# Optimization experiments

Hardware: AMD Instinct MI355X
Metric: run time of the kernel (lower is better)

## Reference

```python
import jax, jax.numpy as jnp
import numpy as np

N = 8192      # number of input points
K = 16        # nsample for all kNN groupings
STRIDE = 4    # TransitionDown stride -> M = N // 4 output points


def _knn(q, p, k):
    # squared euclidean distances [m, n] -> k nearest indices per query
    d2 = jnp.sum(q * q, 1)[:, None] + jnp.sum(p * p, 1)[None, :] - 2.0 * (q @ p.T)
    return jax.lax.top_k(-d2, k)[1]


def _forward(points, We1, se1, be1, We2, se2, be2,
             Wq1, Wk1, Wv1, sa1, ba1, Wq2, Wk2, Wv2, sa2, ba2,
             Wtd, sd, bd, Wu1, su1, bu1, Wu2, su2, bu2,
             Wc1, bc1, sc, bc, Wc2, bc2):
    p = points[0]                      # [N, 3]
    n = p.shape[0]
    idx = _knn(p, p, K)                # [N, K] shared xyz-kNN (same coords every layer)

    def edge_conv(x, W, s, b):
        # DGCNN EdgeConv: concat(x_i, x_j - x_i) -> Linear -> BN(affine) -> ReLU -> max_k
        xi = x[:, None, :]
        xj = x[idx]                    # [N, K, C]
        e = jnp.concatenate([jnp.broadcast_to(xi, xj.shape), xj - xi], -1)
        h = jax.nn.relu((e @ W) * s + b)
        return h.max(axis=1)

    def graph_attn(x, Wq, Wk, Wv, s, b):
        q, kk, v = x @ Wq, x @ Wk, x @ Wv
        kj, vj = kk[idx], v[idx]       # [N, K, D]
        logits = jnp.einsum('nd,nkd->nk', q, kj) / jnp.sqrt(jnp.float32(q.shape[-1]))
        a = jax.nn.softmax(logits, axis=-1)
        y = jnp.einsum('nk,nkd->nd', a, vj)
        return jax.nn.relu(y * s + b)

    x = edge_conv(p, We1, se1, be1)            # 3 -> 64
    x = edge_conv(x, We2, se2, be2)            # 64 -> 128
    x = graph_attn(x, Wq1, Wk1, Wv1, sa1, ba1) # 128 -> 256
    x = graph_attn(x, Wq2, Wk2, Wv2, sa2, ba2) # 256 -> 512

    # TransitionDown: subsample n/stride points, group kNN with relative xyz, MLP, max-pool
    sel = jnp.arange(0, n, STRIDE)
    pm = p[sel]                                 # [M, 3]
    idx_d = _knn(pm, p, K)                      # [M, K]
    g = jnp.concatenate([p[idx_d] - pm[:, None, :], x[idx_d]], -1)  # [M, K, 3+512]
    xd = jax.nn.relu((g @ Wtd) * sd + bd).max(axis=1)               # [M, 512]

    # TransitionUp(x, o): local linear + broadcast per-cloud pooled branch (single cloud, o=[n])
    gmean = xd.mean(axis=0, keepdims=True)
    xu = jax.nn.relu((xd @ Wu1) * su1 + bu1 + (gmean @ Wu2) * su2 + bu2)  # [M, 256]

    # classifier (eval mode: dropout = identity, BN folded to affine)
    h = jax.nn.relu(((xu @ Wc1) + bc1) * sc + bc)
    return h @ Wc2 + bc2               # [M, num_classes]


def setup_inputs() -> dict:
    key = jax.random.key(0)
    ks = iter(jax.random.split(key, 64))
    def w(shape):
        return jax.random.normal(next(ks), shape, jnp.float32) / jnp.sqrt(jnp.float32(shape[0]))
    def s(d):
        return 1.0 + 0.01 * jax.random.normal(next(ks), (d,), jnp.float32)
    def b(d):
        return 0.01 * jax.random.normal(next(ks), (d,), jnp.float32)
    return {
        'points': jax.random.normal(next(ks), (1, N, 3), jnp.float32),
        'We1': w((6, 64)), 'se1': s(64), 'be1': b(64),
        'We2': w((128, 128)), 'se2': s(128), 'be2': b(128),
        'Wq1': w((128, 256)), 'Wk1': w((128, 256)), 'Wv1': w((128, 256)), 'sa1': s(256), 'ba1': b(256),
        'Wq2': w((256, 512)), 'Wk2': w((256, 512)), 'Wv2': w((256, 512)), 'sa2': s(512), 'ba2': b(512),
        'Wtd': w((515, 512)), 'sd': s(512), 'bd': b(512),
        'Wu1': w((512, 256)), 'su1': s(256), 'bu1': b(256),
        'Wu2': w((512, 256)), 'su2': s(256), 'bu2': b(256),
        'Wc1': w((256, 128)), 'bc1': b(128), 'sc': s(128), 'bc': b(128),
        'Wc2': w((128, 6)), 'bc2': b(6),
    }


def reference(points, We1, se1, be1, We2, se2, be2,
              Wq1, Wk1, Wv1, sa1, ba1, Wq2, Wk2, Wv2, sa2, ba2,
              Wtd, sd, bd, Wu1, su1, bu1, Wu2, su2, bu2,
              Wc1, bc1, sc, bc, Wc2, bc2):
    return _forward(points, We1, se1, be1, We2, se2, be2,
                    Wq1, Wk1, Wv1, sa1, ba1, Wq2, Wk2, Wv2, sa2, ba2,
                    Wtd, sd, bd, Wu1, su1, bu1, Wu2, su2, bu2,
                    Wc1, bc1, sc, bc, Wc2, bc2)
```

## Files before the change

### kernel.cpp

```cpp
#include <hip/hip_runtime.h>


#define NP 8192
#define NDOWN 2048
#define KCAP 48

typedef unsigned long long u64;
typedef __attribute__((ext_vector_type(8))) _Float16 half8;
typedef __attribute__((ext_vector_type(4))) unsigned short us4;
typedef __attribute__((ext_vector_type(8))) unsigned short ushort8;
typedef __attribute__((ext_vector_type(4))) float f32x4;

__device__ __forceinline__ bool lexless(float ad, int ai, float bd, int bi) {
  return ad < bd || (ad == bd && ai < bi);
}

__device__ __forceinline__ unsigned short f2h(float x) {
  _Float16 h = (_Float16)x;
  return __builtin_bit_cast(unsigned short, h);
}
__device__ __forceinline__ float h2f(unsigned short u) {
  return (float)__builtin_bit_cast(_Float16, u);
}

__global__ __launch_bounds__(256) void prep_points_k(const float* __restrict__ pts,
                                                     float4* __restrict__ soa) {
  int i = blockIdx.x * 256 + threadIdx.x;
  float x = pts[3 * i], y = pts[3 * i + 1], z = pts[3 * i + 2];
  soa[i] = make_float4(x, y, z, x * x + y * y + z * z);
}

__global__ __launch_bounds__(256) void wsplit_k(
    const float* __restrict__ We2, const float* __restrict__ Wq1,
    const float* __restrict__ Wk1, const float* __restrict__ Wv1,
    const float* __restrict__ Wq2, const float* __restrict__ Wk2,
    const float* __restrict__ Wv2, const float* __restrict__ Wtd,
    const float* __restrict__ Wu1, const float* __restrict__ Wc1,
    unsigned short* __restrict__ whi) {
  int t = blockIdx.x * 256 + threadIdx.x;
  float v;
  if (t < 16384) {
    int n = t >> 6, k = t & 63;
    if (n < 128) v = We2[k * 128 + n] - We2[(k + 64) * 128 + n];
    else         v = We2[(k + 64) * 128 + (n - 128)];
  } else if (t < 114688) {
    int e = t - 16384;
    int n = e >> 7, k = e & 127;
    if (n < 256)      v = Wq1[k * 256 + n];
    else if (n < 512) v = Wk1[k * 256 + (n - 256)];
    else              v = Wv1[k * 256 + (n - 512)];
  } else if (t < 507904) {
    int e = t - 114688;
    int n = e >> 8, k = e & 255;
    if (n < 512)       v = Wq2[k * 512 + n];
    else if (n < 1024) v = Wk2[k * 512 + (n - 512)];
    else               v = Wv2[k * 512 + (n - 1024)];
  } else if (t < 770048) {
    int e = t - 507904;
    int n = e >> 9, k = e & 511;
    v = Wtd[(3 + k) * 512 + n];
  } else if (t < 901120) {
    int e = t - 770048;
    int n = e >> 9, k = e & 511;
    v = Wu1[k * 256 + n];
  } else {
    int e = t - 901120;
    int n = e >> 8, k = e & 255;
    v = Wc1[k * 128 + n];
  }
  whi[t] = f2h(v);
}

__device__ __forceinline__ void bitonic_lex64(float& d, int& i, int lane) {
#pragma unroll
  for (int k = 2; k <= 64; k <<= 1) {
#pragma unroll
    for (int j = k >> 1; j >= 1; j >>= 1) {
      float od = __shfl_xor(d, j);
      int oi = __shfl_xor(i, j);
      bool takeMin = (((lane & k) == 0) == ((lane & j) == 0));
      bool less = lexless(od, oi, d, i);
      if (takeMin == less) { d = od; i = oi; }
    }
  }
}

__device__ __forceinline__ void insert1(float cd, int ci, int lane,
                                        float& td, int& ti) {
  int p = __popcll(__ballot(lexless(td, ti, cd, ci)));
  if (p < 16) {
    float ud = __shfl_up(td, 1);
    int ui = __shfl_up(ti, 1);
    float ntd = td; int nti = ti;
    if (lane > p && lane < 16) { ntd = ud; nti = ui; }
    if (lane == p) { ntd = cd; nti = ci; }
    td = ntd; ti = nti;
  }
}

__global__ __launch_bounds__(512) void knn_k(const float4* __restrict__ soa,
                                             int* __restrict__ idxout) {
  __shared__ float4 sp[2048];
  __shared__ float cb_d[8][KCAP];
  __shared__ int cb_i[8][KCAP];
  __shared__ int ccnt[8];
  const int lane = threadIdx.x & 63;
  const int wid = threadIdx.x >> 6;
  const int q = blockIdx.x * 8 + wid;
  const float4 qp = soa[q];
  const float qx2 = -2.f * qp.x, qy2 = -2.f * qp.y, qz2 = -2.f * qp.z;
  const float INF = __int_as_float(0x7f800000);
  if (lane == 0) ccnt[wid] = 0;

  float md = INF;
  int mi = 0x7fffffff;
  for (int ch = 0; ch < 4; ++ch) {
    __syncthreads();
    for (int j = 0; j < 4; ++j) {
      int e = j * 512 + threadIdx.x;
      sp[e] = soa[ch * 2048 + e];
    }
    __syncthreads();
#pragma unroll 4
    for (int c = 0; c < 32; ++c) {
      const float4 P = sp[c * 64 + lane];
      float m = fmaf(qx2, P.x, qp.w);
      m = fmaf(qy2, P.y, m);
      m = fmaf(qz2, P.z, m);
      const float d = m + P.w;
      const int gidx = ch * 2048 + c * 64 + lane;
      if (d < md) { md = d; mi = gidx; }
    }
  }
  const int own = mi;
  float sd = md; int si = mi;
  bitonic_lex64(sd, si, lane);

  float td = (lane < 16) ? sd : INF;
  int ti = (lane < 16) ? si : 0x7fffffff;
  float Td = __shfl(sd, 15); int Ti = __shfl(si, 15);
  const float tau = Td + fabsf(Td) * 1e-5f + 1e-12f;

  for (int ch = 0; ch < 4; ++ch) {
    __syncthreads();
    for (int j = 0; j < 4; ++j) {
      int e = j * 512 + threadIdx.x;
      sp[e] = soa[ch * 2048 + e];
    }
    __syncthreads();
#pragma unroll 4
    for (int c = 0; c < 32; ++c) {
      const float4 P = sp[c * 64 + lane];
      float m = fmaf(qx2, P.x, qp.w);
      m = fmaf(qy2, P.y, m);
      m = fmaf(qz2, P.z, m);
      const float d = m + P.w;
      const int gidx = ch * 2048 + c * 64 + lane;
      if (d <= tau && gidx != own) {
        int slot = atomicAdd(&ccnt[wid], 1);
        if (slot < KCAP) { cb_d[wid][slot] = d; cb_i[wid][slot] = gidx; }
      }
    }
  }
  int n = ccnt[wid];
  if (n > KCAP) {
    for (int base = 0; base < 8192; base += 64) {
      const float4 P = soa[base + lane];
      float m = fmaf(qx2, P.x, qp.w);
      m = fmaf(qy2, P.y, m);
      m = fmaf(qz2, P.z, m);
      const float d = m + P.w;
      const int gidx = base + lane;
      u64 mk = __ballot(d <= tau && gidx != own && lexless(d, gidx, Td, Ti));
      while (mk) {
        int s = (int)__builtin_ctzll(mk);
        mk &= mk - 1;
        float cd = __shfl(d, s);
        int ci = __shfl(gidx, s);
        insert1(cd, ci, lane, td, ti);
      }
      Td = __shfl(td, 15); Ti = __shfl(ti, 15);
    }
  } else {
    for (int k2 = 0; k2 < n; ++k2) {
      float cd = cb_d[wid][k2];
      int ci = cb_i[wid][k2];
      if (lexless(cd, ci, Td, Ti)) {
        insert1(cd, ci, lane, td, ti);
        Td = __shfl(td, 15); Ti = __shfl(ti, 15);
      }
    }
  }
  if (lane < 16) idxout[q * 16 + lane] = ti & 8191;
}

__global__ __launch_bounds__(256) void proj1_k(const float4* __restrict__ soa,
                                               const float* __restrict__ We1,
                                               float* __restrict__ bz1) {
  int t = blockIdx.x * 256 + threadIdx.x;
  int i = t >> 7, c = t & 127;
  float4 P = soa[i];
  float v;
  if (c < 64) {
    v = P.x * (We1[c] - We1[192 + c]) + P.y * (We1[64 + c] - We1[256 + c]) +
        P.z * (We1[128 + c] - We1[320 + c]);
  } else {
    int cc = c & 63;
    v = P.x * We1[192 + cc] + P.y * We1[256 + cc] + P.z * We1[320 + cc];
  }
  bz1[t] = v;
}

template <int C>
__global__ __launch_bounds__(256) void ec_gm_k(const float* __restrict__ bz,
                                               const int* __restrict__ idx,
                                               const float* __restrict__ s,
                                               const float* __restrict__ b,
                                               unsigned short* __restrict__ xo) {
  constexpr int C4 = C / 4;
  int t = blockIdx.x * 256 + threadIdx.x;
  int i = t / C4, q = t % C4;
  float4 base = *(const float4*)&bz[(size_t)i * (2 * C) + q * 4];
  float4 scl = *(const float4*)&s[q * 4];
  float4 bia = *(const float4*)&b[q * 4];
  float ax = 0.f, ay = 0.f, az = 0.f, aw = 0.f;
  const int* ip = idx + i * 16;
#pragma unroll
  for (int n = 0; n < 16; ++n) {
    int j = ip[n];
    float4 z = *(const float4*)&bz[(size_t)j * (2 * C) + C + q * 4];
    ax = fmaxf(ax, (base.x + z.x) * scl.x + bia.x);
    ay = fmaxf(ay, (base.y + z.y) * scl.y + bia.y);
    az = fmaxf(az, (base.z + z.z) * scl.z + bia.z);
    aw = fmaxf(aw, (base.w + z.w) * scl.w + bia.w);
  }
  us4 o;
  o[0] = f2h(ax); o[1] = f2h(ay); o[2] = f2h(az); o[3] = f2h(aw);
  *(us4*)&xo[(size_t)i * C + q * 4] = o;
}

template <int C>
__global__ __launch_bounds__(256) void attn_logits_k(const float* __restrict__ qf,
                                                     const unsigned short* __restrict__ kvb,
                                                     const int* __restrict__ idx,
                                                     float* __restrict__ aout,
                                                     float scale) {
  int i = blockIdx.x * 4 + (threadIdx.x >> 6);
  int lane = threadIdx.x & 63;
  constexpr int G = C / 256;
  float4 qv[G];
#pragma unroll
  for (int g = 0; g < G; ++g)
    qv[g] = *(const float4*)&qf[(size_t)i * C + 4 * lane + 256 * g];
  float lg[16];
#pragma unroll
  for (int n = 0; n < 16; ++n) {
    int j = idx[i * 16 + n];
    const unsigned short* kr = kvb + (size_t)j * (2 * C);
    float ssum = 0.f;
#pragma unroll
    for (int g = 0; g < G; ++g) {
      us4 kk = *(const us4*)&kr[4 * lane + 256 * g];
      ssum += qv[g].x * h2f(kk[0]) + qv[g].y * h2f(kk[1]) +
              qv[g].z * h2f(kk[2]) + qv[g].w * h2f(kk[3]);
    }
    lg[n] = ssum;
  }
#pragma unroll
  for (int n = 0; n < 16; ++n) {
    float vv = lg[n];
    for (int o = 32; o >= 1; o >>= 1) vv += __shfl_xor(vv, o);
    lg[n] = vv * scale;
  }
  float m = lg[0];
#pragma unroll
  for (int n = 1; n < 16; ++n) m = fmaxf(m, lg[n]);
  float ssum = 0.f;
#pragma unroll
  for (int n = 0; n < 16; ++n) { lg[n] = __expf(lg[n] - m); ssum += lg[n]; }
  float inv = 1.f / ssum;
  if (lane == 0) {
#pragma unroll
    for (int n = 0; n < 16; ++n) aout[i * 16 + n] = lg[n] * inv;
  }
}

template <int C>
__global__ __launch_bounds__(256) void attn_apply_k(const unsigned short* __restrict__ kvb,
                                                    const int* __restrict__ idx,
                                                    const float* __restrict__ awp,
                                                    const float* __restrict__ s,
                                                    const float* __restrict__ b,
                                                    unsigned short* __restrict__ xo) {
  constexpr int C4 = C / 4;
  int t = blockIdx.x * 256 + threadIdx.x;
  int i = t / C4, q = t % C4;
  float ax = 0.f, ay = 0.f, az = 0.f, aw2 = 0.f;
  const int* ip = idx + i * 16;
  const float* ap = awp + i * 16;
#pragma unroll
  for (int n = 0; n < 16; ++n) {
    int j = ip[n];
    float w = ap[n];
    us4 v4 = *(const us4*)&kvb[(size_t)j * (2 * C) + C + 4 * q];
    ax += w * h2f(v4[0]); ay += w * h2f(v4[1]);
    az += w * h2f(v4[2]); aw2 += w * h2f(v4[3]);
  }
  float4 scl = *(const float4*)&s[q * 4];
  float4 bia = *(const float4*)&b[q * 4];
  ax = fmaxf(ax * scl.x + bia.x, 0.f);
  ay = fmaxf(ay * scl.y + bia.y, 0.f);
  az = fmaxf(az * scl.z + bia.z, 0.f);
  aw2 = fmaxf(aw2 * scl.w + bia.w, 0.f);
  us4 o;
  o[0] = f2h(ax); o[1] = f2h(ay); o[2] = f2h(az); o[3] = f2h(aw2);
  *(us4*)&xo[(size_t)i * C + q * 4] = o;
}

__global__ __launch_bounds__(256) void down_gm_k(const float* __restrict__ vbuf,
                                                 const float4* __restrict__ soa,
                                                 const float* __restrict__ Wtd,
                                                 const int* __restrict__ idx,
                                                 const float* __restrict__ sd,
                                                 const float* __restrict__ bd,
                                                 unsigned short* __restrict__ xd) {
  int t = blockIdx.x * 256 + threadIdx.x;
  int i = t >> 7, q = t & 127;
  int qi = 4 * i;
  float4 qp = soa[qi];
  float4 w0 = *(const float4*)&Wtd[q * 4];
  float4 w1 = *(const float4*)&Wtd[512 + q * 4];
  float4 w2 = *(const float4*)&Wtd[1024 + q * 4];
  float px = qp.x * w0.x + qp.y * w1.x + qp.z * w2.x;
  float py = qp.x * w0.y + qp.y * w1.y + qp.z * w2.y;
  float pz = qp.x * w0.z + qp.y * w1.z + qp.z * w2.z;
  float pw2 = qp.x * w0.w + qp.y * w1.w + qp.z * w2.w;
  float4 scl = *(const float4*)&sd[q * 4];
  float4 bia = *(const float4*)&bd[q * 4];
  float ax = 0.f, ay = 0.f, az = 0.f, aw = 0.f;
  const int* ip = idx + qi * 16;
#pragma unroll
  for (int n = 0; n < 16; ++n) {
    int j = ip[n];
    float4 v = *(const float4*)&vbuf[(size_t)j * 512 + q * 4];
    ax = fmaxf(ax, (v.x - px) * scl.x + bia.x);
    ay = fmaxf(ay, (v.y - py) * scl.y + bia.y);
    az = fmaxf(az, (v.z - pz) * scl.z + bia.z);
    aw = fmaxf(aw, (v.w - pw2) * scl.w + bia.w);
  }
  us4 o;
  o[0] = f2h(ax); o[1] = f2h(ay); o[2] = f2h(az); o[3] = f2h(aw);
  *(us4*)&xd[(size_t)i * 512 + q * 4] = o;
}

__global__ __launch_bounds__(512) void colsum_k(const unsigned short* __restrict__ xd,
                                                float* __restrict__ part) {
  int b = blockIdx.x;
  int c = threadIdx.x;
  float s = 0.f;
  for (int r = b * 128; r < (b + 1) * 128; ++r) s += h2f(xd[(size_t)r * 512 + c]);
  part[b * 512 + c] = s;
}

__global__ __launch_bounds__(256) void gterm_k(const float* __restrict__ part,
                                               const float* __restrict__ Wu2,
                                               const float* __restrict__ su2,
                                               const float* __restrict__ bu2,
                                               float* __restrict__ gterm) {
  __shared__ float gm[512];
  int tid = threadIdx.x;
  for (int c = tid; c < 512; c += 256) {
    float s = 0.f;
#pragma unroll
    for (int b = 0; b < 16; ++b) s += part[b * 512 + c];
    gm[c] = s * (1.f / 2048.f);
  }
  __syncthreads();
  float s = 0.f;
  for (int c = 0; c < 512; ++c) s += gm[c] * Wu2[c * 256 + tid];
  gterm[tid] = s * su2[tid] + bu2[tid];
}

#define LDSROW 80
template <int MODE>
__global__ __launch_bounds__(256) void gemm_mfma(
    const unsigned short* __restrict__ A,
    const unsigned short* __restrict__ B,
    float* __restrict__ Cf, unsigned short* __restrict__ Ch,
    int M, int N, int K,
    const float4* __restrict__ soaD, const float* __restrict__ wtd,
    const float* __restrict__ s1, const float* __restrict__ b1,
    const float* __restrict__ s2, int Cq, unsigned short* __restrict__ kvb) {
  __shared__ __align__(16) char smem[2 * 128 * LDSROW];
  char* A_s = smem;
  char* B_s = smem + 128 * LDSROW;

  const int tid = threadIdx.x;
  const int lane = tid & 63;
  const int wid = tid >> 6;
  const int wm = wid >> 1, wn = wid & 1;
  const int bm = blockIdx.y * 128, bn = blockIdx.x * 128;
  const int r16 = lane & 15, kb = lane >> 4;

  f32x4 acc[4][4];
#pragma unroll
  for (int a = 0; a < 4; ++a)
#pragma unroll
    for (int b = 0; b < 4; ++b) acc[a][b] = (f32x4)(0.f);

  for (int k0 = 0; k0 < K; k0 += 32) {
    __syncthreads();
#pragma unroll
    for (int qq = 0; qq < 2; ++qq) {
      int idx8 = qq * 256 + tid;
      int row = idx8 >> 2, sq = idx8 & 3;
      size_t goA = (size_t)(bm + row) * K + k0 + sq * 8;
      size_t goB = (size_t)(bn + row) * K + k0 + sq * 8;
      ushort8 a_v = *(const ushort8*)&A[goA];
      ushort8 b_v = *(const ushort8*)&B[goB];
      *(ushort8*)(A_s + row * LDSROW + sq * 16) = a_v;
      *(ushort8*)(B_s + row * LDSROW + sq * 16) = b_v;
    }
    __syncthreads();

    half8 ah[4];
#pragma unroll
    for (int mi = 0; mi < 4; ++mi) {
      int off = (wm * 64 + mi * 16 + r16) * LDSROW + kb * 16;
      ah[mi] = *(const half8*)(A_s + off);
    }
#pragma unroll
    for (int ni = 0; ni < 4; ++ni) {
      int off = (wn * 64 + ni * 16 + r16) * LDSROW + kb * 16;
      half8 bh = *(const half8*)(B_s + off);
#pragma unroll
      for (int mi = 0; mi < 4; ++mi) {
        acc[mi][ni] = __builtin_amdgcn_mfma_f32_16x16x32_f16(ah[mi], bh, acc[mi][ni], 0, 0, 0);
      }
    }
  }

#pragma unroll
  for (int mi = 0; mi < 4; ++mi) {
#pragma unroll
    for (int ni = 0; ni < 4; ++ni) {
      int r0 = bm + wm * 64 + mi * 16 + (lane >> 4) * 4;
      int cc = bn + wn * 64 + ni * 16 + (lane & 15);
      float w0 = 0.f, w1 = 0.f, w2 = 0.f;
      if (MODE == 1) { w0 = wtd[cc]; w1 = wtd[512 + cc]; w2 = wtd[1024 + cc]; }
#pragma unroll
      for (int j = 0; j < 4; ++j) {
        float vv = acc[mi][ni][j];
        int row = r0 + j;
        if (MODE == 1) {
          float4 P = soaD[row];
          vv += P.x * w0 + P.y * w1 + P.z * w2;
        }
        if (MODE == 2) vv = fmaxf(vv * s1[cc] + b1[cc] + s2[cc], 0.f);
        if (MODE == 3) vv = fmaxf((vv + b1[cc]) * s1[cc] + s2[cc], 0.f);
        if (MODE == 2) {
          Ch[(size_t)row * N + cc] = f2h(vv);
        } else if (MODE == 4) {
          if (cc < Cq) Cf[(size_t)row * Cq + cc] = vv;
          else kvb[(size_t)row * (2 * Cq) + (cc - Cq)] = f2h(vv);
        } else {
          Cf[(size_t)row * N + cc] = vv;
        }
      }
    }
  }
}

__global__ __launch_bounds__(256) void out_k(const float* __restrict__ h,
                                             const float* __restrict__ Wc2,
                                             const float* __restrict__ bc2,
                                             float* __restrict__ out) {
  int t = blockIdx.x * 256 + threadIdx.x;
  int pair = t >> 2, kq = t & 3;
  int i = pair / 6, o = pair % 6;
  float s = 0.f;
#pragma unroll 8
  for (int m = kq * 32; m < kq * 32 + 32; ++m) s += h[i * 128 + m] * Wc2[m * 6 + o];
  s += __shfl_xor(s, 1);
  s += __shfl_xor(s, 2);
  if (kq == 0) out[pair] = s + bc2[o];
}

extern "C" void kernel_launch(void* const* d_in, const int* in_sizes, int n_in,
                              void* d_out, int out_size, void* d_ws, size_t ws_size,
                              hipStream_t stream) {
  const float* pts = (const float*)d_in[0];
  const float* We1 = (const float*)d_in[1];
  const float* se1 = (const float*)d_in[2];
  const float* be1 = (const float*)d_in[3];
  const float* We2 = (const float*)d_in[4];
  const float* se2 = (const float*)d_in[5];
  const float* be2 = (const float*)d_in[6];
  const float* Wq1 = (const float*)d_in[7];
  const float* Wk1 = (const float*)d_in[8];
  const float* Wv1 = (const float*)d_in[9];
  const float* sa1 = (const float*)d_in[10];
  const float* ba1 = (const float*)d_in[11];
  const float* Wq2 = (const float*)d_in[12];
  const float* Wk2 = (const float*)d_in[13];
  const float* Wv2 = (const float*)d_in[14];
  const float* sa2 = (const float*)d_in[15];
  const float* ba2 = (const float*)d_in[16];
  const float* Wtd = (const float*)d_in[17];
  const float* sd  = (const float*)d_in[18];
  const float* bd  = (const float*)d_in[19];
  const float* Wu1 = (const float*)d_in[20];
  const float* su1 = (const float*)d_in[21];
  const float* bu1 = (const float*)d_in[22];
  const float* Wu2 = (const float*)d_in[23];
  const float* su2 = (const float*)d_in[24];
  const float* bu2 = (const float*)d_in[25];
  const float* Wc1 = (const float*)d_in[26];
  const float* bc1 = (const float*)d_in[27];
  const float* sc  = (const float*)d_in[28];
  const float* bc  = (const float*)d_in[29];
  const float* Wc2 = (const float*)d_in[30];
  const float* bc2 = (const float*)d_in[31];

  float* ws = (float*)d_ws;
  if (ws_size < (size_t)16703744 * 4) return;
  float* soa   = ws;
  int*   idx   = (int*)(ws + 32768);
  float* attw  = ws + 163840;
  float* gpart = ws + 294912;
  float* gterm = ws + 303104;
  unsigned short* wthi = (unsigned short*)(ws + 303360);
  unsigned short* x1   = (unsigned short*)(ws + 1237248);
  unsigned short* x2   = (unsigned short*)(ws + 1499392);
  unsigned short* x3   = (unsigned short*)(ws + 2023680);
  unsigned short* x4   = (unsigned short*)(ws + 3072256);
  unsigned short* xd   = (unsigned short*)(ws + 5169408);
  unsigned short* xu   = (unsigned short*)(ws + 5693696);
  float* bufP  = ws + 5955840;
  float* qf    = ws + 8052992;
  unsigned short* kvb = (unsigned short*)(ws + 12247296);
  float* hbuf  = ws + 16441600;

  prep_points_k<<<32, 256, 0, stream>>>(pts, (float4*)soa);
  wsplit_k<<<3648, 256, 0, stream>>>(We2, Wq1, Wk1, Wv1, Wq2, Wk2, Wv2, Wtd, Wu1, Wc1, wthi);
  knn_k<<<1024, 512, 0, stream>>>((const float4*)soa, idx);

  proj1_k<<<4096, 256, 0, stream>>>((const float4*)soa, We1, bufP);
  ec_gm_k<64><<<512, 256, 0, stream>>>(bufP, idx, se1, be1, x1);

  gemm_mfma<0><<<dim3(2, 64), 256, 0, stream>>>(x1, wthi,
      bufP, nullptr, NP, 256, 64, nullptr, nullptr, nullptr, nullptr, nullptr, 0, nullptr);
  ec_gm_k<128><<<1024, 256, 0, stream>>>(bufP, idx, se2, be2, x2);

  gemm_mfma<4><<<dim3(6, 64), 256, 0, stream>>>(x2, wthi + 16384,
      qf, nullptr, NP, 768, 128, nullptr, nullptr, nullptr, nullptr, nullptr, 256, kvb);
  attn_logits_k<256><<<2048, 256, 0, stream>>>(qf, kvb, idx, attw, 0.0625f);
  attn_apply_k<256><<<2048, 256, 0, stream>>>(kvb, idx, attw, sa1, ba1, x3);

  gemm_mfma<4><<<dim3(12, 64), 256, 0, stream>>>(x3, wthi + 114688,
      qf, nullptr, NP, 1536, 256, nullptr, nullptr, nullptr, nullptr, nullptr, 512, kvb);
  attn_logits_k<512><<<2048, 256, 0, stream>>>(qf, kvb, idx, attw, 0.04419417382415922f);
  attn_apply_k<512><<<4096, 256, 0, stream>>>(kvb, idx, attw, sa2, ba2, x4);

  gemm_mfma<1><<<dim3(4, 64), 256, 0, stream>>>(x4, wthi + 507904,
      qf, nullptr, NP, 512, 512, (const float4*)soa, Wtd, nullptr, nullptr, nullptr, 0, nullptr);
  down_gm_k<<<1024, 256, 0, stream>>>(qf, (const float4*)soa, Wtd, idx, sd, bd, xd);

  colsum_k<<<16, 512, 0, stream>>>(xd, gpart);
  gterm_k<<<1, 256, 0, stream>>>(gpart, Wu2, su2, bu2, gterm);

  gemm_mfma<2><<<dim3(2, 16), 256, 0, stream>>>(xd, wthi + 770048,
      nullptr, xu, NDOWN, 256, 512, nullptr, nullptr, su1, bu1, gterm, 0, nullptr);
  gemm_mfma<3><<<dim3(1, 16), 256, 0, stream>>>(xu, wthi + 901120,
      hbuf, nullptr, NDOWN, 128, 256, nullptr, nullptr, sc, bc1, bc, 0, nullptr);
  out_k<<<192, 256, 0, stream>>>(hbuf, Wc2, bc2, (float*)d_out);
}
```

Measured before the change: 264.8 us.

## Simplify kNN selection, fuse attention logits/apply, parallelize gterm reduction

```diff
diff --git a/kernel.cpp b/kernel.cpp
--- a/kernel.cpp
+++ b/kernel.cpp
@@ -3,7 +3,7 @@
 
 #define NP 8192
 #define NDOWN 2048
-#define KCAP 48
+#define KCAP 64
 
 typedef unsigned long long u64;
 typedef __attribute__((ext_vector_type(8))) _Float16 half8;
@@ -71,6 +71,18 @@
   whi[t] = f2h(v);
 }
 
+__device__ __forceinline__ void bitonic_val64(float& d, int lane) {
+#pragma unroll
+  for (int k = 2; k <= 64; k <<= 1) {
+#pragma unroll
+    for (int j = k >> 1; j >= 1; j >>= 1) {
+      float od = __shfl_xor(d, j);
+      bool takeMin = (((lane & k) == 0) == ((lane & j) == 0));
+      d = takeMin ? fminf(d, od) : fmaxf(d, od);
+    }
+  }
+}
+
 __device__ __forceinline__ void bitonic_lex64(float& d, int& i, int lane) {
 #pragma unroll
   for (int k = 2; k <= 64; k <<= 1) {
@@ -113,7 +125,27 @@
   if (lane == 0) ccnt[wid] = 0;
 
   float md = INF;
-  int mi = 0x7fffffff;
+  for (int ch = 0; ch < 4; ++ch) {
+    __syncthreads();
+    for (int j = 0; j < 4; ++j) {
+      int e = j * 512 + threadIdx.x;
+      sp[e] = soa[ch * 2048 + e];
+    }
+    __syncthreads();
+#pragma unroll 4
+    for (int c = 0; c < 32; ++c) {
+      const float4 P = sp[c * 64 + lane];
+      float m = fmaf(qx2, P.x, qp.w);
+      m = fmaf(qy2, P.y, m);
+      m = fmaf(qz2, P.z, m);
+      md = fminf(md, m + P.w);
+    }
+  }
+  float sv = md;
+  bitonic_val64(sv, lane);
+  const float tau = __shfl(sv, 15);
+  const float tauM = tau + fabsf(tau) * 1e-5f + 1e-12f;
+
   for (int ch = 0; ch < 4; ++ch) {
     __syncthreads();
     for (int j = 0; j < 4; ++j) {
@@ -128,42 +160,24 @@
       m = fmaf(qy2, P.y, m);
       m = fmaf(qz2, P.z, m);
       const float d = m + P.w;
-      const int gidx = ch * 2048 + c * 64 + lane;
-      if (d < md) { md = d; mi = gidx; }
-    }
-  }
-  const int own = mi;
-  float sd = md; int si = mi;
-  bitonic_lex64(sd, si, lane);
-
-  float td = (lane < 16) ? sd : INF;
-  int ti = (lane < 16) ? si : 0x7fffffff;
-  float Td = __shfl(sd, 15); int Ti = __shfl(si, 15);
-  const float tau = Td + fabsf(Td) * 1e-5f + 1e-12f;
-
-  for (int ch = 0; ch < 4; ++ch) {
-    __syncthreads();
-    for (int j = 0; j < 4; ++j) {
-      int e = j * 512 + threadIdx.x;
-      sp[e] = soa[ch * 2048 + e];
-    }
-    __syncthreads();
-#pragma unroll 4
-    for (int c = 0; c < 32; ++c) {
-      const float4 P = sp[c * 64 + lane];
-      float m = fmaf(qx2, P.x, qp.w);
-      m = fmaf(qy2, P.y, m);
-      m = fmaf(qz2, P.z, m);
-      const float d = m + P.w;
-      const int gidx = ch * 2048 + c * 64 + lane;
-      if (d <= tau && gidx != own) {
+      if (d <= tauM) {
         int slot = atomicAdd(&ccnt[wid], 1);
-        if (slot < KCAP) { cb_d[wid][slot] = d; cb_i[wid][slot] = gidx; }
+        if (slot < KCAP) {
+          cb_d[wid][slot] = d;
+          cb_i[wid][slot] = ch * 2048 + c * 64 + lane;
+        }
       }
     }
   }
   int n = ccnt[wid];
-  if (n > KCAP) {
+  if (n <= KCAP) {
+    float dd = (lane < n) ? cb_d[wid][lane] : INF;
+    int ii = (lane < n) ? cb_i[wid][lane] : 0x7fffffff;
+    bitonic_lex64(dd, ii, lane);
+    if (lane < 16) idxout[q * 16 + lane] = ii & 8191;
+  } else {
+    float td = INF; int ti = 0x7fffffff;
+    float Td = INF; int Ti = 0x7fffffff;
     for (int base = 0; base < 8192; base += 64) {
       const float4 P = soa[base + lane];
       float m = fmaf(qx2, P.x, qp.w);
@@ -171,7 +185,7 @@
       m = fmaf(qz2, P.z, m);
       const float d = m + P.w;
       const int gidx = base + lane;
-      u64 mk = __ballot(d <= tau && gidx != own && lexless(d, gidx, Td, Ti));
+      u64 mk = __ballot(d <= tauM && lexless(d, gidx, Td, Ti));
       while (mk) {
         int s = (int)__builtin_ctzll(mk);
         mk &= mk - 1;
@@ -181,17 +195,8 @@
       }
       Td = __shfl(td, 15); Ti = __shfl(ti, 15);
     }
-  } else {
-    for (int k2 = 0; k2 < n; ++k2) {
-      float cd = cb_d[wid][k2];
-      int ci = cb_i[wid][k2];
-      if (lexless(cd, ci, Td, Ti)) {
-        insert1(cd, ci, lane, td, ti);
-        Td = __shfl(td, 15); Ti = __shfl(ti, 15);
-      }
-    }
-  }
-  if (lane < 16) idxout[q * 16 + lane] = ti & 8191;
+    if (lane < 16) idxout[q * 16 + lane] = ti & 8191;
+  }
 }
 
 __global__ __launch_bounds__(256) void proj1_k(const float4* __restrict__ soa,
@@ -240,14 +245,17 @@
 }
 
 template <int C>
-__global__ __launch_bounds__(256) void attn_logits_k(const float* __restrict__ qf,
-                                                     const unsigned short* __restrict__ kvb,
-                                                     const int* __restrict__ idx,
-                                                     float* __restrict__ aout,
-                                                     float scale) {
+__global__ __launch_bounds__(256) void attn_fused_k(const float* __restrict__ qf,
+                                                    const unsigned short* __restrict__ kvb,
+                                                    const int* __restrict__ idx,
+                                                    const float* __restrict__ s,
+                                                    const float* __restrict__ b,
+                                                    unsigned short* __restrict__ xo,
+                                                    float scale) {
   int i = blockIdx.x * 4 + (threadIdx.x >> 6);
   int lane = threadIdx.x & 63;
   constexpr int G = C / 256;
+  int jreg = (lane < 16) ? idx[i * 16 + lane] : 0;
   float4 qv[G];
 #pragma unroll
   for (int g = 0; g < G; ++g)
@@ -255,7 +263,7 @@
   float lg[16];
 #pragma unroll
   for (int n = 0; n < 16; ++n) {
-    int j = idx[i * 16 + n];
+    int j = __shfl(jreg, n);
     const unsigned short* kr = kvb + (size_t)j * (2 * C);
     float ssum = 0.f;
 #pragma unroll
@@ -279,42 +287,38 @@
 #pragma unroll
   for (int n = 0; n < 16; ++n) { lg[n] = __expf(lg[n] - m); ssum += lg[n]; }
   float inv = 1.f / ssum;
-  if (lane == 0) {
-#pragma unroll
-    for (int n = 0; n < 16; ++n) aout[i * 16 + n] = lg[n] * inv;
-  }
-}
-
-template <int C>
-__global__ __launch_bounds__(256) void attn_apply_k(const unsigned short* __restrict__ kvb,
-                                                    const int* __restrict__ idx,
-                                                    const float* __restrict__ awp,
-                                                    const float* __restrict__ s,
-                                                    const float* __restrict__ b,
-                                                    unsigned short* __restrict__ xo) {
-  constexpr int C4 = C / 4;
-  int t = blockIdx.x * 256 + threadIdx.x;
-  int i = t / C4, q = t % C4;
-  float ax = 0.f, ay = 0.f, az = 0.f, aw2 = 0.f;
-  const int* ip = idx + i * 16;
-  const float* ap = awp + i * 16;
+#pragma unroll
+  for (int n = 0; n < 16; ++n) lg[n] *= inv;
+
+  float acc[4 * G];
+#pragma unroll
+  for (int e = 0; e < 4 * G; ++e) acc[e] = 0.f;
 #pragma unroll
   for (int n = 0; n < 16; ++n) {
-    int j = ip[n];
-    float w = ap[n];
-    us4 v4 = *(const us4*)&kvb[(size_t)j * (2 * C) + C + 4 * q];
-    ax += w * h2f(v4[0]); ay += w * h2f(v4[1]);
-    az += w * h2f(v4[2]); aw2 += w * h2f(v4[3]);
-  }
-  float4 scl = *(const float4*)&s[q * 4];
-  float4 bia = *(const float4*)&b[q * 4];
-  ax = fmaxf(ax * scl.x + bia.x, 0.f);
-  ay = fmaxf(ay * scl.y + bia.y, 0.f);
-  az = fmaxf(az * scl.z + bia.z, 0.f);
-  aw2 = fmaxf(aw2 * scl.w + bia.w, 0.f);
-  us4 o;
-  o[0] = f2h(ax); o[1] = f2h(ay); o[2] = f2h(az); o[3] = f2h(aw2);
-  *(us4*)&xo[(size_t)i * C + q * 4] = o;
+    int j = __shfl(jreg, n);
+    const unsigned short* vr = kvb + (size_t)j * (2 * C) + C;
+    float w = lg[n];
+#pragma unroll
+    for (int g = 0; g < G; ++g) {
+      us4 v4 = *(const us4*)&vr[4 * lane + 256 * g];
+      acc[4 * g + 0] += w * h2f(v4[0]);
+      acc[4 * g + 1] += w * h2f(v4[1]);
+      acc[4 * g + 2] += w * h2f(v4[2]);
+      acc[4 * g + 3] += w * h2f(v4[3]);
+    }
+  }
+#pragma unroll
+  for (int g = 0; g < G; ++g) {
+    int c0 = 4 * lane + 256 * g;
+    float4 scl = *(const float4*)&s[c0];
+    float4 bia = *(const float4*)&b[c0];
+    us4 o;
+    o[0] = f2h(fmaxf(acc[4 * g + 0] * scl.x + bia.x, 0.f));
+    o[1] = f2h(fmaxf(acc[4 * g + 1] * scl.y + bia.y, 0.f));
+    o[2] = f2h(fmaxf(acc[4 * g + 2] * scl.z + bia.z, 0.f));
+    o[3] = f2h(fmaxf(acc[4 * g + 3] * scl.w + bia.w, 0.f));
+    *(us4*)&xo[(size_t)i * C + c0] = o;
+  }
 }
 
 __global__ __launch_bounds__(256) void down_gm_k(const float* __restrict__ vbuf,
@@ -376,9 +380,16 @@
     gm[c] = s * (1.f / 2048.f);
   }
   __syncthreads();
+  int o = blockIdx.x * 16 + (tid >> 4);
+  int kseg = tid & 15;
   float s = 0.f;
-  for (int c = 0; c < 512; ++c) s += gm[c] * Wu2[c * 256 + tid];
-  gterm[tid] = s * su2[tid] + bu2[tid];
+#pragma unroll 8
+  for (int k = kseg * 32; k < kseg * 32 + 32; ++k) s += gm[k] * Wu2[k * 256 + o];
+  s += __shfl_xor(s, 1);
+  s += __shfl_xor(s, 2);
+  s += __shfl_xor(s, 4);
+  s += __shfl_xor(s, 8);
+  if (kseg == 0) gterm[o] = s * su2[o] + bu2[o];
 }
 
 #define LDSROW 80
@@ -526,7 +537,6 @@
   if (ws_size < (size_t)16703744 * 4) return;
   float* soa   = ws;
   int*   idx   = (int*)(ws + 32768);
-  float* attw  = ws + 163840;
   float* gpart = ws + 294912;
   float* gterm = ws + 303104;
   unsigned short* wthi = (unsigned short*)(ws + 303360);
@@ -554,20 +564,18 @@
 
   gemm_mfma<4><<<dim3(6, 64), 256, 0, stream>>>(x2, wthi + 16384,
       qf, nullptr, NP, 768, 128, nullptr, nullptr, nullptr, nullptr, nullptr, 256, kvb);
-  attn_logits_k<256><<<2048, 256, 0, stream>>>(qf, kvb, idx, attw, 0.0625f);
-  attn_apply_k<256><<<2048, 256, 0, stream>>>(kvb, idx, attw, sa1, ba1, x3);
+  attn_fused_k<256><<<2048, 256, 0, stream>>>(qf, kvb, idx, sa1, ba1, x3, 0.0625f);
 
   gemm_mfma<4><<<dim3(12, 64), 256, 0, stream>>>(x3, wthi + 114688,
       qf, nullptr, NP, 1536, 256, nullptr, nullptr, nullptr, nullptr, nullptr, 512, kvb);
-  attn_logits_k<512><<<2048, 256, 0, stream>>>(qf, kvb, idx, attw, 0.04419417382415922f);
-  attn_apply_k<512><<<4096, 256, 0, stream>>>(kvb, idx, attw, sa2, ba2, x4);
+  attn_fused_k<512><<<2048, 256, 0, stream>>>(qf, kvb, idx, sa2, ba2, x4, 0.04419417382415922f);
 
   gemm_mfma<1><<<dim3(4, 64), 256, 0, stream>>>(x4, wthi + 507904,
       qf, nullptr, NP, 512, 512, (const float4*)soa, Wtd, nullptr, nullptr, nullptr, 0, nullptr);
   down_gm_k<<<1024, 256, 0, stream>>>(qf, (const float4*)soa, Wtd, idx, sd, bd, xd);
 
   colsum_k<<<16, 512, 0, stream>>>(xd, gpart);
-  gterm_k<<<1, 256, 0, stream>>>(gpart, Wu2, su2, bu2, gterm);
+  gterm_k<<<16, 256, 0, stream>>>(gpart, Wu2, su2, bu2, gterm);
 
   gemm_mfma<2><<<dim3(2, 16), 256, 0, stream>>>(xd, wthi + 770048,
       nullptr, xu, NDOWN, 256, 512, nullptr, nullptr, su1, bu1, gterm, 0, nullptr);
```

Measured after the change: 266.6 us. About the same (+0.7%).
